# Optimization experiments

Measured on AMD Instinct MI355X. Metric: run time of the kernel, lower is better.

Reference implementation:

```python
import jax, jax.numpy as jnp
import numpy as np

TAU = 2.0
V_TH = 1.0
SG_ALPHA = 4.0  # spikingjelly default sigmoid surrogate alpha
BN_EPS = 1e-5

@jax.custom_vjp
def spike_fn(v):
    return (v >= V_TH).astype(v.dtype)

def _spike_fwd(v):
    return spike_fn(v), v

def _spike_bwd(v, g):
    s = jax.nn.sigmoid(SG_ALPHA * (v - V_TH))
    return (g * SG_ALPHA * s * (1.0 - s),)

spike_fn.defvjp(_spike_fwd, _spike_bwd)

def lif(x):
    """Multi-step LIF, tau=2, hard reset to 0, detach_reset. x: (T, ...)."""
    def step(v, xt):
        v = v + (xt - v) / TAU
        s = spike_fn(v)
        v = v * (1.0 - jax.lax.stop_gradient(s))
        return v, s
    _, spikes = jax.lax.scan(step, jnp.zeros_like(x[0]), x)
    return spikes

def batchnorm1d(x, gamma, beta):
    """Training-mode BatchNorm1d over channel dim. x: (N, C, L)."""
    mean = jnp.mean(x, axis=(0, 2), keepdims=True)
    var = jnp.var(x, axis=(0, 2), keepdims=True)  # biased, as torch uses for normalization
    xhat = (x - mean) * jax.lax.rsqrt(var + BN_EPS)
    return xhat * gamma[None, :, None] + beta[None, :, None]

def setup_inputs() -> dict:
    key = jax.random.key(0)
    k_x, k_w1, k_w2 = jax.random.split(key, 3)
    T, B, L, D, H = 4, 64, 64, 768, 3072
    x = jax.random.normal(k_x, (T, B, L, D), dtype=jnp.float32)
    W1 = jax.random.normal(k_w1, (H, D), dtype=jnp.float32) / np.sqrt(D)
    gamma1 = jnp.ones((H,), dtype=jnp.float32)
    beta1 = jnp.zeros((H,), dtype=jnp.float32)
    W2 = jax.random.normal(k_w2, (D, H), dtype=jnp.float32) / np.sqrt(H)
    gamma2 = jnp.ones((D,), dtype=jnp.float32)
    beta2 = jnp.zeros((D,), dtype=jnp.float32)
    return {"x": x, "W1": W1, "gamma1": gamma1, "beta1": beta1,
            "W2": W2, "gamma2": gamma2, "beta2": beta2}

def reference(x, W1, gamma1, beta1, W2, gamma2, beta2):
    T, B, L, D = x.shape
    H = W1.shape[0]
    # --- block 1 ---
    s = lif(x)                                        # (T,B,L,D)
    h = jnp.einsum('tbld,hd->tblh', s, W1)            # (T,B,L,H)
    h = batchnorm1d(h.reshape(T * B, L, H).transpose(0, 2, 1), gamma1, beta1)  # (T*B,H,L)
    # faithful quirk: reshape WITHOUT transposing back
    h = h.reshape(T, B, L, H)
    # --- block 2 ---
    s2 = lif(h)                                       # (T,B,L,H)
    o = jnp.einsum('tblh,dh->tbld', s2, W2)           # (T,B,L,D)
    o = batchnorm1d(o.reshape(T * B, L, D).transpose(0, 2, 1), gamma2, beta2)  # (T*B,D,L)
    o = o.reshape(T, B, L, D)
    return o
```

## Files before the change

kernel.cpp:

```cpp
#include <hip/hip_runtime.h>
#include <stdint.h>
#include <stddef.h>

#define T_ 4
#define B_ 64
#define L_ 64
#define D_ 768
#define H_ 3072
#define M1_ 16384
#define BLD_ 3145728
#define NW_ 2359296
#define HL_ 196608

using f4    = __attribute__((ext_vector_type(4))) float;
using int4v = __attribute__((ext_vector_type(4))) int;
using uc4   = __attribute__((ext_vector_type(4))) unsigned char;
using uc16  = __attribute__((ext_vector_type(16))) unsigned char;
using ui2   = __attribute__((ext_vector_type(2))) unsigned int;

static __device__ __forceinline__ void gload_lds16(const void* g, void* l) {
  __builtin_amdgcn_global_load_lds((const __attribute__((address_space(1))) void*)g,
                                   (__attribute__((address_space(3))) void*)l, 16, 0, 0);
}

#define SGB() __builtin_amdgcn_sched_barrier(0)
#define HWBAR() __builtin_amdgcn_s_barrier()

#define INV33 (1.0/8589934592.0)

__global__ __launch_bounds__(256) void k_convert(
    const float* __restrict__ W1, const float* __restrict__ W2,
    signed char* __restrict__ Q0, signed char* __restrict__ Q1,
    signed char* __restrict__ Q2, signed char* __restrict__ Q3,
    int* __restrict__ Qint,
    signed char* __restrict__ R0, signed char* __restrict__ R1) {
  int i = blockIdx.x * 256 + threadIdx.x;
  if (i >= NW_) return;
  {
    double w = (double)W1[i];
    long long q = llrint(w * 8589934592.0);
    if (q >  2113929216LL) q =  2113929216LL;
    if (q < -2113929216LL) q = -2113929216LL;
    int ii = (int)q;
    Qint[i] = ii;
    int b0 = ((ii + 128) & 255) - 128; ii = (ii - b0) >> 8;
    int b1 = ((ii + 128) & 255) - 128; ii = (ii - b1) >> 8;
    int b2 = ((ii + 128) & 255) - 128; ii = (ii - b2) >> 8;
    Q0[i] = (signed char)b0; Q1[i] = (signed char)b1;
    Q2[i] = (signed char)b2; Q3[i] = (signed char)ii;
  }
  {
    double w = (double)W2[i];
    long long q = llrint(w * 131072.0);
    if (q >  32512LL) q =  32512LL;
    if (q < -32512LL) q = -32512LL;
    int ii = (int)q;
    int b0 = ((ii + 128) & 255) - 128;
    R0[i] = (signed char)b0;
    R1[i] = (signed char)((ii - b0) >> 8);
  }
}

__global__ __launch_bounds__(256) void k_lif1(const float* __restrict__ x,
                                              unsigned char* __restrict__ s1) {
  size_t i = ((size_t)blockIdx.x * 256 + threadIdx.x) * 4;
  double v0 = 0., v1 = 0., v2 = 0., v3 = 0.;
  #pragma unroll
  for (int t = 0; t < T_; ++t) {
    f4 xt = *(const f4*)(x + (size_t)t * BLD_ + i);
    v0 = v0 + ((double)xt.x - v0) * 0.5;
    v1 = v1 + ((double)xt.y - v1) * 0.5;
    v2 = v2 + ((double)xt.z - v2) * 0.5;
    v3 = v3 + ((double)xt.w - v3) * 0.5;
    uc4 s;
    s.x = (v0 >= 1.0) ? 1 : 0;
    s.y = (v1 >= 1.0) ? 1 : 0;
    s.z = (v2 >= 1.0) ? 1 : 0;
    s.w = (v3 >= 1.0) ? 1 : 0;
    *(uc4*)(s1 + (size_t)t * BLD_ + i) = s;
    v0 = s.x ? 0. : v0;
    v1 = s.y ? 0. : v1;
    v2 = s.z ? 0. : v2;
    v3 = s.w ? 0. : v3;
  }
}

__global__ __launch_bounds__(256) void k_s1t(const unsigned char* __restrict__ s1,
                                             unsigned char* __restrict__ sT,
                                             int* __restrict__ colsum) {
  __shared__ __align__(16) unsigned char sm[64 * 80];
  const int tid = threadIdx.x;
  const int d0 = blockIdx.x * 64;
  const int bl0 = blockIdx.y * 64;
  const int t = blockIdx.z;
  {
    const int i = tid >> 2, ch = tid & 3;
    uc16 v = *(const uc16*)(s1 + (size_t)t * BLD_ + (size_t)(bl0 + i) * 768 + d0 + ch * 16);
    *(uc16*)(sm + i * 80 + ch * 16) = v;
  }
  __syncthreads();
  {
    const int d = tid >> 2, oc = tid & 3;
    union { uc16 v; unsigned char b[16]; } u;
    int s = 0;
    #pragma unroll
    for (int jj = 0; jj < 16; ++jj) {
      unsigned char c = sm[(oc * 16 + jj) * 80 + d];
      u.b[jj] = c;
      s += c;
    }
    *(uc16*)(sT + (size_t)(d0 + d) * M1_ + t * 4096 + bl0 + oc * 16) = u.v;
    s += __shfl_xor(s, 1);
    s += __shfl_xor(s, 2);
    if ((tid & 3) == 0) atomicAdd(&colsum[d0 + d], s);
  }
}

__global__ __launch_bounds__(256, 2) void k_gram(const unsigned char* __restrict__ sT,
                                                 int* __restrict__ Gpart) {
  __shared__ __align__(16) char smem[32768];
  const int tid = threadIdx.x;
  const int lane = tid & 63;
  const int wr = tid >> 7;
  const int wc = (tid >> 6) & 1;
  const int tr = blockIdx.x / 6, tc = blockIdx.x % 6;
  const int ks = blockIdx.y;
  const size_t m0 = (size_t)ks * 2048;

  const int s0 = tid, s1i = tid + 256;
  const int rA0 = s0 >> 2, rA1 = s1i >> 2;
  const int cA0 = (s0 & 3) ^ ((rA0 >> 1) & 3);
  const int cA1 = (s1i & 3) ^ ((rA1 >> 1) & 3);
  const unsigned char* Ag0 = sT + (size_t)(tr * 128 + rA0) * M1_ + m0 + cA0 * 16;
  const unsigned char* Ag1 = sT + (size_t)(tr * 128 + rA1) * M1_ + m0 + cA1 * 16;
  const unsigned char* Bg0 = sT + (size_t)(tc * 128 + rA0) * M1_ + m0 + cA0 * 16;
  const unsigned char* Bg1 = sT + (size_t)(tc * 128 + rA1) * M1_ + m0 + cA1 * 16;

  int4v acc[4][4] = {};
  const int clog = lane >> 4;

  gload_lds16(Ag0, smem + s0 * 16);
  gload_lds16(Ag1, smem + s1i * 16);
  gload_lds16(Bg0, smem + 8192 + s0 * 16);
  gload_lds16(Bg1, smem + 8192 + s1i * 16);
  __syncthreads();

  for (int kt = 0; kt < 32; ++kt) {
    if (kt < 31) {
      const int kn = (kt + 1) * 64;
      char* dst = smem + ((kt + 1) & 1) * 16384;
      gload_lds16(Ag0 + kn, dst + s0 * 16);
      gload_lds16(Ag1 + kn, dst + s1i * 16);
      gload_lds16(Bg0 + kn, dst + 8192 + s0 * 16);
      gload_lds16(Bg1 + kn, dst + 8192 + s1i * 16);
    }
    const signed char* ldsA = (const signed char*)smem + (kt & 1) * 16384;
    const signed char* ldsB = ldsA + 8192;
    int4v av[4], bv[4];
    #pragma unroll
    for (int m = 0; m < 4; ++m) {
      const int r = wr * 64 + m * 16 + (lane & 15);
      const int cp = clog ^ ((r >> 1) & 3);
      av[m] = *(const int4v*)(ldsA + r * 64 + cp * 16);
    }
    #pragma unroll
    for (int n = 0; n < 4; ++n) {
      const int r = wc * 64 + n * 16 + (lane & 15);
      const int cp = clog ^ ((r >> 1) & 3);
      bv[n] = *(const int4v*)(ldsB + r * 64 + cp * 16);
    }
    #pragma unroll
    for (int m = 0; m < 4; ++m)
      #pragma unroll
      for (int n = 0; n < 4; ++n)
        acc[m][n] = __builtin_amdgcn_mfma_i32_16x16x64_i8(av[m], bv[n], acc[m][n], 0, 0, 0);
    __syncthreads();
  }

  const int r0 = tr * 128 + wr * 64 + (clog << 2);
  const int c0 = tc * 128 + wc * 64 + (lane & 15);
  #pragma unroll
  for (int m = 0; m < 4; ++m)
    #pragma unroll
    for (int n = 0; n < 4; ++n)
      #pragma unroll
      for (int rr = 0; rr < 4; ++rr)
        Gpart[((size_t)ks * 768 + r0 + m * 16 + rr) * 768 + c0 + n * 16] = acc[m][n][rr];
}

__global__ __launch_bounds__(256) void k_gramred(const int* __restrict__ Gpart,
                                                 signed char* __restrict__ g0,
                                                 signed char* __restrict__ g1) {
  int i = blockIdx.x * 256 + threadIdx.x;
  if (i >= 768 * 768) return;
  int G = 0;
  #pragma unroll
  for (int ks = 0; ks < 8; ++ks) G += Gpart[(size_t)ks * 768 * 768 + i];
  int b0 = ((G + 128) & 255) - 128;
  g0[i] = (signed char)b0;
  g1[i] = (signed char)((G - b0) >> 8);
}

__global__ __launch_bounds__(256, 2) void k_gq(
    const signed char* __restrict__ g0, const signed char* __restrict__ g1,
    const signed char* __restrict__ Q0, const signed char* __restrict__ Q1,
    const signed char* __restrict__ Q2, const signed char* __restrict__ Q3,
    double* __restrict__ YT) {
  __shared__ __align__(16) char smem[49152];
  const int tid = threadIdx.x;
  const int lane = tid & 63;
  const int w = tid >> 6;
  const int k0 = blockIdx.x * 64;
  const int c0 = blockIdx.y * 64;

  const int row = tid >> 2;
  const int ch = (tid & 3) ^ ((row >> 1) & 3);
  const signed char* Ag[2] = { g0 + (size_t)(k0 + row) * 768 + ch * 16,
                               g1 + (size_t)(k0 + row) * 768 + ch * 16 };
  const signed char* Bg[4] = { Q0 + (size_t)(c0 + row) * 768 + ch * 16,
                               Q1 + (size_t)(c0 + row) * 768 + ch * 16,
                               Q2 + (size_t)(c0 + row) * 768 + ch * 16,
                               Q3 + (size_t)(c0 + row) * 768 + ch * 16 };

  int4v acc[8][4] = {};
  const int clog = lane >> 4;

  #pragma unroll
  for (int a = 0; a < 2; ++a) gload_lds16(Ag[a], smem + a * 4096 + tid * 16);
  #pragma unroll
  for (int p = 0; p < 4; ++p) gload_lds16(Bg[p], smem + 8192 + p * 4096 + tid * 16);
  __syncthreads();

  for (int kt = 0; kt < 12; ++kt) {
    if (kt < 11) {
      const int kn = (kt + 1) * 64;
      char* dst = smem + ((kt + 1) & 1) * 24576;
      #pragma unroll
      for (int a = 0; a < 2; ++a) gload_lds16(Ag[a] + kn, dst + a * 4096 + tid * 16);
      #pragma unroll
      for (int p = 0; p < 4; ++p) gload_lds16(Bg[p] + kn, dst + 8192 + p * 4096 + tid * 16);
    }
    const signed char* base = (const signed char*)smem + (kt & 1) * 24576;
    const int ar = w * 16 + (lane & 15);
    const int acp = clog ^ ((ar >> 1) & 3);
    int4v av[2];
    #pragma unroll
    for (int a = 0; a < 2; ++a)
      av[a] = *(const int4v*)(base + a * 4096 + ar * 64 + acp * 16);
    #pragma unroll
    for (int p = 0; p < 4; ++p) {
      int4v bv[4];
      #pragma unroll
      for (int n = 0; n < 4; ++n) {
        const int br = n * 16 + (lane & 15);
        const int bcp = clog ^ ((br >> 1) & 3);
        bv[n] = *(const int4v*)(base + 8192 + p * 4096 + br * 64 + bcp * 16);
      }
      #pragma unroll
      for (int a = 0; a < 2; ++a)
        #pragma unroll
        for (int n = 0; n < 4; ++n)
          acc[a * 4 + p][n] = __builtin_amdgcn_mfma_i32_16x16x64_i8(av[a], bv[n], acc[a * 4 + p][n], 0, 0, 0);
    }
    __syncthreads();
  }

  #pragma unroll
  for (int n = 0; n < 4; ++n)
    #pragma unroll
    for (int r = 0; r < 4; ++r) {
      int A0 = acc[0][n][r] + (acc[4][n][r] << 8);
      int A1 = acc[1][n][r] + (acc[5][n][r] << 8);
      int A2 = acc[2][n][r] + (acc[6][n][r] << 8);
      int A3 = acc[3][n][r] + (acc[7][n][r] << 8);
      double Y = (double)A0 + 256.0 * (double)A1 + 65536.0 * (double)A2 + 16777216.0 * (double)A3;
      const int k = k0 + w * 16 + clog * 4 + r;
      const int c = c0 + n * 16 + (lane & 15);
      YT[(size_t)c * 768 + k] = Y;
    }
}

__global__ __launch_bounds__(256) void k_stats1(
    const double* __restrict__ YT, const int* __restrict__ Qint,
    const int* __restrict__ colsum,
    double* __restrict__ mean, double* __restrict__ rstd) {
  __shared__ double red[8];
  const int c = blockIdx.x;
  const int tid = threadIdx.x;
  double s2 = 0.0, sm = 0.0;
  for (int k = tid; k < 768; k += 256) {
    double q = (double)Qint[(size_t)c * 768 + k];
    s2 += q * YT[(size_t)c * 768 + k];
    sm += q * (double)colsum[k];
  }
  #pragma unroll
  for (int o = 32; o; o >>= 1) { s2 += __shfl_xor(s2, o); sm += __shfl_xor(sm, o); }
  if ((tid & 63) == 0) { red[(tid >> 6) * 2] = s2; red[(tid >> 6) * 2 + 1] = sm; }
  __syncthreads();
  if (tid == 0) {
    double S2 = red[0] + red[2] + red[4] + red[6];
    double SM = red[1] + red[3] + red[5] + red[7];
    double mn = SM * INV33 * (1.0 / 16384.0);
    double Eh2 = S2 * INV33 * INV33 * (1.0 / 16384.0);
    double var = Eh2 - mn * mn;
    mean[c] = mn;
    rstd[c] = 1.0 / sqrt(var + 1e-5);
  }
}

__global__ __launch_bounds__(256, 2) void k_bnlif(
    const unsigned char* __restrict__ A,
    const signed char* __restrict__ Q0, const signed char* __restrict__ Q1,
    const signed char* __restrict__ Q2, const signed char* __restrict__ Q3,
    const double* __restrict__ mean, const double* __restrict__ rstd,
    const float* __restrict__ gamma, const float* __restrict__ beta,
    signed char* __restrict__ s2) {
  __shared__ __align__(16) char smem[73728];
  const int tid  = threadIdx.x;
  const int lane = tid & 63;
  const int w    = tid >> 6;
  const int wr = tid >> 7;
  const int wc = (tid >> 6) & 1;
  const int n0 = blockIdx.x * 64;
  const int by = blockIdx.y;

  auto grow = [&](int r) -> size_t {
    return (size_t)4096 * (r >> 5) + (size_t)by * 32 + (r & 31);
  };
  const int aIdx0 = w * 128 + lane;
  const int aIdx1 = aIdx0 + 64;
  const int ar0 = aIdx0 >> 2, ar1 = aIdx1 >> 2;
  const int ac0 = (aIdx0 & 3) ^ ((ar0 >> 1) & 3);
  const int ac1 = (aIdx1 & 3) ^ ((ar1 >> 1) & 3);
  const unsigned char* Ag0 = A + grow(ar0) * 768 + ac0 * 16;
  const unsigned char* Ag1 = A + grow(ar1) * 768 + ac1 * 16;
  const int bIdx = w * 64 + lane;
  const int brS = bIdx >> 2;
  const int bcS = (bIdx & 3) ^ ((brS >> 1) & 3);
  const signed char* Bg[4] = { Q0 + (size_t)(n0 + brS) * 768 + bcS * 16,
                               Q1 + (size_t)(n0 + brS) * 768 + bcS * 16,
                               Q2 + (size_t)(n0 + brS) * 768 + bcS * 16,
                               Q3 + (size_t)(n0 + brS) * 768 + bcS * 16 };

  int4v acc[4][4][2] = {};
  const int arow = wr * 64 + (lane & 15);
  const int clog = lane >> 4;

  auto stage = [&](int t) {
    char* dst = smem + (t % 3) * 24576;
    const int kn = t * 64;
    gload_lds16(Ag0 + kn, dst + aIdx0 * 16);
    gload_lds16(Ag1 + kn, dst + aIdx1 * 16);
    #pragma unroll
    for (int p = 0; p < 4; ++p) gload_lds16(Bg[p] + kn, dst + 8192 + p * 4096 + bIdx * 16);
  };

  stage(0);
  stage(1);
  for (int kt = 0; kt < 12; ++kt) {
    if (kt <= 9) stage(kt + 2);
    if (kt <= 9)       { asm volatile("s_waitcnt vmcnt(12)" ::: "memory"); }
    else if (kt == 10) { asm volatile("s_waitcnt vmcnt(6)" ::: "memory"); }
    else               { asm volatile("s_waitcnt vmcnt(0)" ::: "memory"); }
    SGB();
    HWBAR();
    SGB();
    const signed char* ldsA = (const signed char*)smem + (kt % 3) * 24576;
    const signed char* ldsB = ldsA + 8192;
    int4v av[4], bv[2][4];
    #pragma unroll
    for (int m = 0; m < 4; ++m) {
      const int r = arow + m * 16;
      const int cp = clog ^ ((r >> 1) & 3);
      av[m] = *(const int4v*)(ldsA + r * 64 + cp * 16);
    }
    #pragma unroll
    for (int n = 0; n < 2; ++n) {
      const int r = wc * 32 + n * 16 + (lane & 15);
      const int cp = clog ^ ((r >> 1) & 3);
      #pragma unroll
      for (int p = 0; p < 4; ++p)
        bv[n][p] = *(const int4v*)(ldsB + p * 4096 + r * 64 + cp * 16);
    }
    #pragma unroll
    for (int p = 0; p < 4; ++p)
      #pragma unroll
      for (int m = 0; m < 4; ++m)
        #pragma unroll
        for (int n = 0; n < 2; ++n)
          acc[p][m][n] = __builtin_amdgcn_mfma_i32_16x16x64_i8(av[m], bv[n][p], acc[p][m][n], 0, 0, 0);
    SGB();
    HWBAR();
  }

  unsigned int* smLo = (unsigned int*)smem;
  short*        smHi = (short*)(smem + 32768);
  #pragma unroll
  for (int m = 0; m < 4; ++m)
    #pragma unroll
    for (int n = 0; n < 2; ++n)
      #pragma unroll
      for (int r = 0; r < 4; ++r) {
        long long h = ((long long)acc[3][m][n][r] << 24) + ((long long)acc[2][m][n][r] << 16)
                    + ((long long)acc[1][m][n][r] << 8) + (long long)acc[0][m][n][r];
        const int rw = wr * 64 + m * 16 + clog * 4 + r;
        const int cl = wc * 32 + n * 16 + (lane & 15);
        smLo[rw * 64 + cl] = (unsigned int)h;
        smHi[rw * 64 + cl] = (short)(h >> 32);
      }
  __syncthreads();

  const int col = tid & 63;
  const int jgrp = tid >> 6;
  const int c = n0 + col;
  const double mn = mean[c], rs = rstd[c];
  const double gm = (double)gamma[c], bt = (double)beta[c];
  const int bI = by >> 1;
  const int l0 = (by & 1) * 32;
  unsigned int plo[4] = {0, 0, 0, 0}, phi[4] = {0, 0, 0, 0};
  #pragma unroll
  for (int jj = 0; jj < 8; ++jj) {
    const int j = jgrp * 8 + jj;
    double v = 0.;
    #pragma unroll
    for (int t = 0; t < 4; ++t) {
      const int rw = t * 32 + j;
      long long h = ((long long)smHi[rw * 64 + col] << 32) | (unsigned long long)smLo[rw * 64 + col];
      double g = ((double)h * INV33 - mn) * rs * gm + bt;
      v = v + (g - v) * 0.5;
      bool s = (v >= 1.0);
      if (s) { if (jj < 4) plo[t] |= 1u << (8 * jj); else phi[t] |= 1u << (8 * (jj - 4)); }
      v = s ? 0. : v;
    }
  }
  #pragma unroll
  for (int t = 0; t < 4; ++t) {
    ui2 wv; wv.x = plo[t]; wv.y = phi[t];
    *(ui2*)(s2 + (size_t)(t * 64 + bI) * HL_ + (size_t)c * 64 + l0 + jgrp * 8) = wv;
  }
}

__global__ __launch_bounds__(256, 2) void k_gemm2(
    const signed char* __restrict__ A,
    const signed char* __restrict__ R0, const signed char* __restrict__ R1,
    float* __restrict__ C,
    double* __restrict__ partS, double* __restrict__ partQ) {
  __shared__ __align__(16) char smem[73728];
  const int tid  = threadIdx.x;
  const int lane = tid & 63;
  const int w    = tid >> 6;
  const int wr = tid >> 7;
  const int wc = (tid >> 6) & 1;
  const int n0 = blockIdx.x * 128;
  const int by = blockIdx.y;

  const int i0 = w * 128 + lane;
  const int i1 = i0 + 64;
  const int r0s = i0 >> 2, r1s = i1 >> 2;
  const int c0s = (i0 & 3) ^ ((r0s >> 1) & 3);
  const int c1s = (i1 & 3) ^ ((r1s >> 1) & 3);
  const signed char* Ag0 = A + (size_t)(by * 128 + r0s) * 3072 + c0s * 16;
  const signed char* Ag1 = A + (size_t)(by * 128 + r1s) * 3072 + c1s * 16;
  const signed char* P0g0 = R0 + (size_t)(n0 + r0s) * 3072 + c0s * 16;
  const signed char* P0g1 = R0 + (size_t)(n0 + r1s) * 3072 + c1s * 16;
  const signed char* P1g0 = R1 + (size_t)(n0 + r0s) * 3072 + c0s * 16;
  const signed char* P1g1 = R1 + (size_t)(n0 + r1s) * 3072 + c1s * 16;

  int4v acc[2][4][4] = {};
  const int arow = wr * 64 + (lane & 15);
  const int brow = wc * 64 + (lane & 15);
  const int clog = lane >> 4;

  auto stage = [&](int t) {
    char* dst = smem + (t % 3) * 24576;
    const int kn = t * 64;
    gload_lds16(Ag0 + kn, dst + i0 * 16);
    gload_lds16(Ag1 + kn, dst + i1 * 16);
    gload_lds16(P0g0 + kn, dst + 8192 + i0 * 16);
    gload_lds16(P0g1 + kn, dst + 8192 + i1 * 16);
    gload_lds16(P1g0 + kn, dst + 16384 + i0 * 16);
    gload_lds16(P1g1 + kn, dst + 16384 + i1 * 16);
  };

  stage(0);
  stage(1);
  for (int kt = 0; kt < 48; ++kt) {
    if (kt <= 45) stage(kt + 2);
    if (kt <= 45)      { asm volatile("s_waitcnt vmcnt(12)" ::: "memory"); }
    else if (kt == 46) { asm volatile("s_waitcnt vmcnt(6)" ::: "memory"); }
    else               { asm volatile("s_waitcnt vmcnt(0)" ::: "memory"); }
    SGB();
    HWBAR();
    SGB();
    const signed char* ldsA = (const signed char*)smem + (kt % 3) * 24576;
    int4v av[4], bv[2][4];
    #pragma unroll
    for (int m = 0; m < 4; ++m) {
      const int r = arow + m * 16;
      const int cp = clog ^ ((r >> 1) & 3);
      av[m] = *(const int4v*)(ldsA + r * 64 + cp * 16);
    }
    #pragma unroll
    for (int n = 0; n < 4; ++n) {
      const int r = brow + n * 16;
      const int cp = clog ^ ((r >> 1) & 3);
      bv[0][n] = *(const int4v*)(ldsA + 8192 + r * 64 + cp * 16);
      bv[1][n] = *(const int4v*)(ldsA + 16384 + r * 64 + cp * 16);
    }
    #pragma unroll
    for (int p = 0; p < 2; ++p)
      #pragma unroll
      for (int m = 0; m < 4; ++m)
        #pragma unroll
        for (int n = 0; n < 4; ++n)
          acc[p][m][n] = __builtin_amdgcn_mfma_i32_16x16x64_i8(av[m], bv[p][n], acc[p][m][n], 0, 0, 0);
    SGB();
    HWBAR();
  }

  const int r0o = by * 128 + wr * 64 + (clog << 2);
  const int c0o = n0 + wc * 64 + (lane & 15);
  #pragma unroll
  for (int n = 0; n < 4; ++n) {
    double s = 0.0, q = 0.0;
    #pragma unroll
    for (int m = 0; m < 4; ++m)
      #pragma unroll
      for (int r = 0; r < 4; ++r) {
        int hv = acc[0][m][n][r] + 256 * acc[1][m][n][r];
        double h = (double)hv * (1.0 / 131072.0);
        C[(size_t)(r0o + m * 16 + r) * 768 + (c0o + n * 16)] = (float)h;
        s += h;
        q += h * h;
      }
    s += __shfl_xor(s, 16);
    q += __shfl_xor(q, 16);
    s += __shfl_xor(s, 32);
    q += __shfl_xor(q, 32);
    if (clog == 0) {
      int col = n0 + wc * 64 + n * 16 + lane;
      partS[(size_t)(by * 2 + wr) * D_ + col] = s;
      partQ[(size_t)(by * 2 + wr) * D_ + col] = q;
    }
  }
}

__global__ __launch_bounds__(256) void k_bnred(
    const double* __restrict__ pS, const double* __restrict__ pQ,
    double* __restrict__ mean, double* __restrict__ rstd, int N, double invM) {
  int i = blockIdx.x * 256 + threadIdx.x;
  if (i >= N) return;
  double s = 0.0, q = 0.0;
  for (int p = 0; p < 256; ++p) {
    s += pS[(size_t)p * N + i];
    q += pQ[(size_t)p * N + i];
  }
  double m = s * invM;
  double v = q * invM - m * m;
  mean[i] = m;
  rstd[i] = 1.0 / sqrt(v + 1e-5);
}

__global__ __launch_bounds__(256) void k_bn2apply(
    const float* __restrict__ O, const double* __restrict__ mean,
    const double* __restrict__ rstd, const float* __restrict__ gamma,
    const float* __restrict__ beta, float* __restrict__ out) {
  __shared__ __align__(16) float sm[64 * 65];
  const int tid = threadIdx.x;
  const int d0 = blockIdx.x * 64;
  const int tb = blockIdx.y;
  const int doff = tid & 63;
  const int lgrp = tid >> 6;
  const double mn = mean[d0 + doff];
  const double rs = rstd[d0 + doff];
  const double gm = (double)gamma[d0 + doff];
  const double bt = (double)beta[d0 + doff];
  #pragma unroll 4
  for (int p = 0; p < 16; ++p) {
    const int l = p * 4 + lgrp;
    double v = (double)O[((size_t)tb * 64 + l) * D_ + d0 + doff];
    sm[doff * 65 + l] = (float)(((v - mn) * rs) * gm + bt);
  }
  __syncthreads();
  const int l4 = (tid & 15) * 4;
  const int db = tid >> 4;
  #pragma unroll
  for (int p = 0; p < 4; ++p) {
    const int dd = p * 16 + db;
    f4 wv;
    wv.x = sm[dd * 65 + l4 + 0];
    wv.y = sm[dd * 65 + l4 + 1];
    wv.z = sm[dd * 65 + l4 + 2];
    wv.w = sm[dd * 65 + l4 + 3];
    *(f4*)(out + (size_t)tb * (D_ * L_) + (size_t)(d0 + dd) * 64 + l4) = wv;
  }
}

extern "C" void kernel_launch(void* const* d_in, const int* in_sizes, int n_in,
                              void* d_out, int out_size, void* d_ws, size_t ws_size,
                              hipStream_t stream) {
  const float* x      = (const float*)d_in[0];
  const float* W1     = (const float*)d_in[1];
  const float* gamma1 = (const float*)d_in[2];
  const float* beta1  = (const float*)d_in[3];
  const float* W2     = (const float*)d_in[4];
  const float* gamma2 = (const float*)d_in[5];
  const float* beta2  = (const float*)d_in[6];
  float* out = (float*)d_out;
  (void)in_sizes; (void)n_in; (void)out_size; (void)ws_size;

  unsigned char* s1 = (unsigned char*)d_out;

  char* ws = (char*)d_ws;
  size_t off = 0;
  auto alloc = [&](size_t bytes) -> void* {
    void* p = ws + off;
    off += (bytes + 255) & ~(size_t)255;
    return p;
  };
  signed char* Q0 = (signed char*)alloc(NW_);
  signed char* Q1 = (signed char*)alloc(NW_);
  signed char* Q2 = (signed char*)alloc(NW_);
  signed char* Q3 = (signed char*)alloc(NW_);
  int* Qint       = (int*)alloc((size_t)NW_ * 4);
  signed char* R0 = (signed char*)alloc(NW_);
  signed char* R1 = (signed char*)alloc(NW_);
  unsigned char* s1T = (unsigned char*)alloc((size_t)768 * M1_);
  int* Gpart      = (int*)alloc((size_t)8 * 768 * 768 * 4);
  signed char* g0 = (signed char*)alloc((size_t)768 * 768);
  signed char* g1 = (signed char*)alloc((size_t)768 * 768);
  double* YT      = (double*)alloc((size_t)H_ * 768 * 8);
  int* colsum     = (int*)alloc(768 * 4);
  signed char* s2 = (signed char*)alloc((size_t)M1_ * H_);
  float* O2       = (float*)alloc((size_t)M1_ * D_ * 4);
  double* pS2 = (double*)alloc((size_t)256 * D_ * 8);
  double* pQ2 = (double*)alloc((size_t)256 * D_ * 8);
  double* mean1 = (double*)alloc((size_t)H_ * 8);
  double* rstd1 = (double*)alloc((size_t)H_ * 8);
  double* mean2 = (double*)alloc((size_t)D_ * 8);
  double* rstd2 = (double*)alloc((size_t)D_ * 8);

  hipMemsetAsync(colsum, 0, 768 * 4, stream);
  k_convert<<<NW_ / 256, 256, 0, stream>>>(W1, W2, Q0, Q1, Q2, Q3, Qint, R0, R1);
  k_lif1<<<BLD_ / 4 / 256, 256, 0, stream>>>(x, s1);
  k_s1t<<<dim3(12, 64, 4), 256, 0, stream>>>(s1, s1T, colsum);
  k_gram<<<dim3(36, 8), 256, 0, stream>>>(s1T, Gpart);
  k_gramred<<<(768 * 768) / 256, 256, 0, stream>>>(Gpart, g0, g1);
  k_gq<<<dim3(12, 48), 256, 0, stream>>>(g0, g1, Q0, Q1, Q2, Q3, YT);
  k_stats1<<<H_, 256, 0, stream>>>(YT, Qint, colsum, mean1, rstd1);
  k_bnlif<<<dim3(H_ / 64, (B_ * L_) / 32), 256, 0, stream>>>(
      s1, Q0, Q1, Q2, Q3, mean1, rstd1, gamma1, beta1, s2);
  k_gemm2<<<dim3(D_ / 128, M1_ / 128), 256, 0, stream>>>(s2, R0, R1, O2, pS2, pQ2);
  k_bnred<<<(D_ + 255) / 256, 256, 0, stream>>>(pS2, pQ2, mean2, rstd2, D_, 1.0 / (double)M1_);
  k_bn2apply<<<dim3(D_ / 64, T_ * B_), 256, 0, stream>>>(O2, mean2, rstd2, gamma2, beta2, out);
}
```

Before: 380.5 us.

## Split k_bnlif byte-plane MFMA work across 512-thread blocks

k_bnlif now launches 512 threads per block. Two wave groups each compute two of the four int8 weight byte-plane products and write packed 32-bit partials to separate LDS buffers, which the epilogue adds into a 64-bit value. Each wave holds half as many accumulators and issues fewer loads per stage, so per-thread register pressure drops and more waves are available to hide latency. The cost is an extra LDS partial buffer and read in the epilogue. LDS use per block (72 KB) likely caps residency below the requested 4 blocks per CU.

```diff
diff --git a/kernel.cpp b/kernel.cpp
--- a/kernel.cpp
+++ b/kernel.cpp
@@ -16,7 +16,6 @@
 using int4v = __attribute__((ext_vector_type(4))) int;
 using uc4   = __attribute__((ext_vector_type(4))) unsigned char;
 using uc16  = __attribute__((ext_vector_type(16))) unsigned char;
-using ui2   = __attribute__((ext_vector_type(2))) unsigned int;
 
 static __device__ __forceinline__ void gload_lds16(const void* g, void* l) {
   __builtin_amdgcn_global_load_lds((const __attribute__((address_space(1))) void*)g,
@@ -308,7 +307,7 @@
   }
 }
 
-__global__ __launch_bounds__(256, 2) void k_bnlif(
+__global__ __launch_bounds__(512, 4) void k_bnlif(
     const unsigned char* __restrict__ A,
     const signed char* __restrict__ Q0, const signed char* __restrict__ Q1,
     const signed char* __restrict__ Q2, const signed char* __restrict__ Q3,
@@ -318,56 +317,51 @@
   __shared__ __align__(16) char smem[73728];
   const int tid  = threadIdx.x;
   const int lane = tid & 63;
-  const int w    = tid >> 6;
-  const int wr = tid >> 7;
-  const int wc = (tid >> 6) & 1;
+  const int wid  = tid >> 6;
+  const int wp = wid & 1;
+  const int wc = (wid >> 1) & 1;
+  const int wr = wid >> 2;
   const int n0 = blockIdx.x * 64;
   const int by = blockIdx.y;
 
   auto grow = [&](int r) -> size_t {
     return (size_t)4096 * (r >> 5) + (size_t)by * 32 + (r & 31);
   };
-  const int aIdx0 = w * 128 + lane;
-  const int aIdx1 = aIdx0 + 64;
-  const int ar0 = aIdx0 >> 2, ar1 = aIdx1 >> 2;
-  const int ac0 = (aIdx0 & 3) ^ ((ar0 >> 1) & 3);
-  const int ac1 = (aIdx1 & 3) ^ ((ar1 >> 1) & 3);
-  const unsigned char* Ag0 = A + grow(ar0) * 768 + ac0 * 16;
-  const unsigned char* Ag1 = A + grow(ar1) * 768 + ac1 * 16;
-  const int bIdx = w * 64 + lane;
-  const int brS = bIdx >> 2;
-  const int bcS = (bIdx & 3) ^ ((brS >> 1) & 3);
-  const signed char* Bg[4] = { Q0 + (size_t)(n0 + brS) * 768 + bcS * 16,
-                               Q1 + (size_t)(n0 + brS) * 768 + bcS * 16,
-                               Q2 + (size_t)(n0 + brS) * 768 + bcS * 16,
-                               Q3 + (size_t)(n0 + brS) * 768 + bcS * 16 };
-
-  int4v acc[4][4][2] = {};
+  const int aRow = tid >> 2;
+  const int aCol = (tid & 3) ^ ((aRow >> 1) & 3);
+  const unsigned char* Ag = A + grow(aRow) * 768 + aCol * 16;
+  const int bSel = (tid >> 8) & 1;
+  const int bi = tid & 255;
+  const int bRow = bi >> 2;
+  const int bCol = (bi & 3) ^ ((bRow >> 1) & 3);
+  const signed char* Bg0 = (bSel ? Q1 : Q0) + (size_t)(n0 + bRow) * 768 + bCol * 16;
+  const signed char* Bg1 = (bSel ? Q3 : Q2) + (size_t)(n0 + bRow) * 768 + bCol * 16;
+
+  int4v acc[2][4][2] = {};
   const int arow = wr * 64 + (lane & 15);
   const int clog = lane >> 4;
 
   auto stage = [&](int t) {
     char* dst = smem + (t % 3) * 24576;
     const int kn = t * 64;
-    gload_lds16(Ag0 + kn, dst + aIdx0 * 16);
-    gload_lds16(Ag1 + kn, dst + aIdx1 * 16);
-    #pragma unroll
-    for (int p = 0; p < 4; ++p) gload_lds16(Bg[p] + kn, dst + 8192 + p * 4096 + bIdx * 16);
+    gload_lds16(Ag + kn, dst + tid * 16);
+    gload_lds16(Bg0 + kn, dst + 8192 + tid * 16);
+    gload_lds16(Bg1 + kn, dst + 8192 + 8192 + tid * 16);
   };
 
   stage(0);
   stage(1);
   for (int kt = 0; kt < 12; ++kt) {
     if (kt <= 9) stage(kt + 2);
-    if (kt <= 9)       { asm volatile("s_waitcnt vmcnt(12)" ::: "memory"); }
-    else if (kt == 10) { asm volatile("s_waitcnt vmcnt(6)" ::: "memory"); }
+    if (kt <= 9)       { asm volatile("s_waitcnt vmcnt(6)" ::: "memory"); }
+    else if (kt == 10) { asm volatile("s_waitcnt vmcnt(3)" ::: "memory"); }
     else               { asm volatile("s_waitcnt vmcnt(0)" ::: "memory"); }
     SGB();
     HWBAR();
     SGB();
     const signed char* ldsA = (const signed char*)smem + (kt % 3) * 24576;
-    const signed char* ldsB = ldsA + 8192;
-    int4v av[4], bv[2][4];
+    const signed char* ldsB = ldsA + 8192 + wp * 8192;
+    int4v av[4], bv[2][2];
     #pragma unroll
     for (int m = 0; m < 4; ++m) {
       const int r = arow + m * 16;
@@ -378,12 +372,11 @@
     for (int n = 0; n < 2; ++n) {
       const int r = wc * 32 + n * 16 + (lane & 15);
       const int cp = clog ^ ((r >> 1) & 3);
-      #pragma unroll
-      for (int p = 0; p < 4; ++p)
-        bv[n][p] = *(const int4v*)(ldsB + p * 4096 + r * 64 + cp * 16);
-    }
-    #pragma unroll
-    for (int p = 0; p < 4; ++p)
+      bv[n][0] = *(const int4v*)(ldsB + r * 64 + cp * 16);
+      bv[n][1] = *(const int4v*)(ldsB + 4096 + r * 64 + cp * 16);
+    }
+    #pragma unroll
+    for (int p = 0; p < 2; ++p)
       #pragma unroll
       for (int m = 0; m < 4; ++m)
         #pragma unroll
@@ -393,20 +386,19 @@
     HWBAR();
   }
 
-  unsigned int* smLo = (unsigned int*)smem;
-  short*        smHi = (short*)(smem + 32768);
+  int* smP0 = (int*)smem;
+  int* smP1 = (int*)(smem + 32768);
+  int* dstP = wp ? smP1 : smP0;
   #pragma unroll
   for (int m = 0; m < 4; ++m)
     #pragma unroll
     for (int n = 0; n < 2; ++n)
       #pragma unroll
       for (int r = 0; r < 4; ++r) {
-        long long h = ((long long)acc[3][m][n][r] << 24) + ((long long)acc[2][m][n][r] << 16)
-                    + ((long long)acc[1][m][n][r] << 8) + (long long)acc[0][m][n][r];
+        const int val = acc[0][m][n][r] + (acc[1][m][n][r] << 8);
         const int rw = wr * 64 + m * 16 + clog * 4 + r;
         const int cl = wc * 32 + n * 16 + (lane & 15);
-        smLo[rw * 64 + cl] = (unsigned int)h;
-        smHi[rw * 64 + cl] = (short)(h >> 32);
+        dstP[rw * 64 + cl] = val;
       }
   __syncthreads();
 
@@ -417,27 +409,25 @@
   const double gm = (double)gamma[c], bt = (double)beta[c];
   const int bI = by >> 1;
   const int l0 = (by & 1) * 32;
-  unsigned int plo[4] = {0, 0, 0, 0}, phi[4] = {0, 0, 0, 0};
-  #pragma unroll
-  for (int jj = 0; jj < 8; ++jj) {
-    const int j = jgrp * 8 + jj;
+  unsigned int pk[4] = {0, 0, 0, 0};
+  #pragma unroll
+  for (int jj = 0; jj < 4; ++jj) {
+    const int j = jgrp * 4 + jj;
     double v = 0.;
     #pragma unroll
     for (int t = 0; t < 4; ++t) {
       const int rw = t * 32 + j;
-      long long h = ((long long)smHi[rw * 64 + col] << 32) | (unsigned long long)smLo[rw * 64 + col];
+      long long h = (long long)smP0[rw * 64 + col] + ((long long)smP1[rw * 64 + col] << 16);
       double g = ((double)h * INV33 - mn) * rs * gm + bt;
       v = v + (g - v) * 0.5;
       bool s = (v >= 1.0);
-      if (s) { if (jj < 4) plo[t] |= 1u << (8 * jj); else phi[t] |= 1u << (8 * (jj - 4)); }
+      if (s) pk[t] |= 1u << (8 * jj);
       v = s ? 0. : v;
     }
   }
   #pragma unroll
-  for (int t = 0; t < 4; ++t) {
-    ui2 wv; wv.x = plo[t]; wv.y = phi[t];
-    *(ui2*)(s2 + (size_t)(t * 64 + bI) * HL_ + (size_t)c * 64 + l0 + jgrp * 8) = wv;
-  }
+  for (int t = 0; t < 4; ++t)
+    *(unsigned int*)(s2 + (size_t)(t * 64 + bI) * HL_ + (size_t)c * 64 + l0 + jgrp * 4) = pk[t];
 }
 
 __global__ __launch_bounds__(256, 2) void k_gemm2(
@@ -648,7 +638,7 @@
   k_gramred<<<(768 * 768) / 256, 256, 0, stream>>>(Gpart, g0, g1);
   k_gq<<<dim3(12, 48), 256, 0, stream>>>(g0, g1, Q0, Q1, Q2, Q3, YT);
   k_stats1<<<H_, 256, 0, stream>>>(YT, Qint, colsum, mean1, rstd1);
-  k_bnlif<<<dim3(H_ / 64, (B_ * L_) / 32), 256, 0, stream>>>(
+  k_bnlif<<<dim3(H_ / 64, (B_ * L_) / 32), 512, 0, stream>>>(
       s1, Q0, Q1, Q2, Q3, mean1, rstd1, gamma1, beta1, s2);
   k_gemm2<<<dim3(D_ / 128, M1_ / 128), 256, 0, stream>>>(s2, R0, R1, O2, pS2, pQ2);
   k_bnred<<<(D_ + 255) / 256, 256, 0, stream>>>(pS2, pQ2, mean2, rstd2, D_, 1.0 / (double)M1_);
```

New measurement: 391.2 us. 2.8% more time.
